# Kernel tuning notes

Hardware: AMD Instinct MI355X
Metric: run time of the kernel (lower is better)

## Reference

```python
import jax, jax.numpy as jnp
import numpy as np

B, N, H = 64, 512, 1024
NH = 8            # attention heads
HD = H // NH      # head dim
STEPS = 24


def setup_inputs() -> dict:
    key = jax.random.key(0)
    ks = jax.random.split(key, 12)
    s = 0.05  # weight scale to keep gates/softmax in a sane range
    return {
        "encoder_outputs": jax.random.normal(ks[0], (B, N, H), dtype=jnp.float32),
        "hidden": jax.random.normal(ks[1], (B, H), dtype=jnp.float32) * s,
        "cell": jax.random.normal(ks[2], (B, H), dtype=jnp.float32) * s,
        "end_node_embed": jax.random.normal(ks[3], (B, H), dtype=jnp.float32),
        "initial_input": jax.random.normal(ks[4], (B, 3 * H), dtype=jnp.float32),
        "max_steps": STEPS,
        # LSTMCell params (torch layout: [4H, in], gate order i,f,g,o)
        "W_ih": jax.random.normal(ks[5], (4 * H, 3 * H), dtype=jnp.float32) * s,
        "b_ih": jnp.zeros((4 * H,), jnp.float32),
        "W_hh": jax.random.normal(ks[6], (4 * H, H), dtype=jnp.float32) * s,
        "b_hh": jnp.zeros((4 * H,), jnp.float32),
        # MultiheadAttention params (torch in_proj [3H,H] = [Wq;Wk;Wv])
        "attn_in_w": jax.random.normal(ks[7], (3 * H, H), dtype=jnp.float32) * s,
        "attn_in_b": jnp.zeros((3 * H,), jnp.float32),
        "attn_out_w": jax.random.normal(ks[8], (H, H), dtype=jnp.float32) * s,
        "attn_out_b": jnp.zeros((H,), jnp.float32),
        # query_transform Linear
        "qt_w": jax.random.normal(ks[9], (H, H), dtype=jnp.float32) * s,
        "qt_b": jnp.zeros((H,), jnp.float32),
    }


def reference(encoder_outputs, hidden, cell, end_node_embed, initial_input,
              max_steps, W_ih, b_ih, W_hh, b_hh,
              attn_in_w, attn_in_b, attn_out_w, attn_out_b, qt_w, qt_b):
    b, n, h = encoder_outputs.shape
    nh, hd = NH, H // NH
    Wq, Wk, Wv = jnp.split(attn_in_w, 3, axis=0)
    bq, bk, bv = jnp.split(attn_in_b, 3)
    S = max_steps
    dt = encoder_outputs.dtype
    buf0 = jnp.zeros((b, S, h), dt)  # preallocated KV cache of decoder hiddens
    neg = jnp.asarray(-1e30, dt)
    scale = 1.0 / jnp.sqrt(jnp.asarray(hd, dt))
    pos = jnp.arange(S)

    def step(carry, t):
        hn, cn, x, buf = carry
        # --- LSTMCell (torch gate order i,f,g,o) ---
        gates = x @ W_ih.T + b_ih + hn @ W_hh.T + b_hh
        i, f, g, o = jnp.split(gates, 4, axis=-1)
        cn = jax.nn.sigmoid(f) * cn + jax.nn.sigmoid(i) * jnp.tanh(g)
        hn = jax.nn.sigmoid(o) * jnp.tanh(cn)
        buf = buf.at[:, t, :].set(hn)
        # --- causal self-attention: q = current hidden, kv = all hiddens <= t ---
        q = (hn @ Wq.T + bq).reshape(b, nh, hd)
        k = (buf @ Wk.T + bk).reshape(b, S, nh, hd)
        v = (buf @ Wv.T + bv).reshape(b, S, nh, hd)
        scores = jnp.einsum('bhd,bshd->bhs', q, k) * scale
        scores = jnp.where((pos > t)[None, None, :], neg, scores)
        attn = jax.nn.softmax(scores, axis=-1)
        ctx = jnp.einsum('bhs,bshd->bhd', attn, v).reshape(b, h)
        attn_out = ctx @ attn_out_w.T + attn_out_b
        # --- pointer scoring ---
        query = (0.5 * (hn + attn_out)) @ qt_w.T + qt_b
        logits = jnp.einsum('bh,bnh->bn', query, encoder_outputs)  # [B,N]
        _, idx = jax.lax.top_k(logits, 3)
        idx = jnp.sort(idx, axis=1)
        top3 = jnp.take_along_axis(encoder_outputs, idx[:, :, None], axis=1)  # [B,3,H]
        x = top3.reshape(b, 3 * h)
        return (hn, cn, x, buf), (logits, idx)

    _, (logits, idx) = jax.lax.scan(
        step, (hidden, cell, initial_input, buf0), jnp.arange(S))
    return logits, idx  # [max_steps,B,N], [max_steps,B,3]
```

## Files before the change

### kernel.cpp

```cpp
#include <hip/hip_runtime.h>
#include <math.h>

#define B_  64
#define N_  512
#define H_  1024
#define NH_ 8
#define HD_ 128
#define S_  24

__global__ __launch_bounds__(256) void wc_pre(
    const float* __restrict__ Wqt, const float* __restrict__ Wout,
    float* __restrict__ W2)
{
  __shared__ float As[16][68];
  __shared__ float Bs[16][68];
  const int tid = threadIdx.x;
  const int k0 = (blockIdx.x & 15) * 64;
  const int n0 = (blockIdx.x >> 4) * 64;
  const int tn = tid & 15, tm = tid >> 4;

#pragma unroll
  for (int i = 0; i < 4; ++i) {
    int n = n0 + tm * 4 + i;
    float4 w = *(const float4*)(Wqt + (size_t)n * 1024 + k0 + tn * 4);
    *(float4*)(W2 + (size_t)n * 2048 + k0 + tn * 4) =
        make_float4(0.5f * w.x, 0.5f * w.y, 0.5f * w.z, 0.5f * w.w);
  }

  float acc[4][4];
#pragma unroll
  for (int i = 0; i < 4; ++i)
#pragma unroll
    for (int j = 0; j < 4; ++j) acc[i][j] = 0.f;

  for (int m0 = 0; m0 < 1024; m0 += 16) {
    {
      int nn = tid >> 2, mm = (tid & 3) * 4;
      float4 a = *(const float4*)(Wqt + (size_t)(n0 + nn) * 1024 + m0 + mm);
      As[mm + 0][nn] = a.x; As[mm + 1][nn] = a.y;
      As[mm + 2][nn] = a.z; As[mm + 3][nn] = a.w;
      int mr = tid >> 4, kc = (tid & 15) * 4;
      float4 b = *(const float4*)(Wout + (size_t)(m0 + mr) * 1024 + k0 + kc);
      *(float4*)(&Bs[mr][kc]) = b;
    }
    __syncthreads();
#pragma unroll
    for (int m = 0; m < 16; ++m) {
      float av[4], bv[4];
      *(float4*)av = *(const float4*)(&As[m][tm * 4]);
      *(float4*)bv = *(const float4*)(&Bs[m][tn * 4]);
#pragma unroll
      for (int i = 0; i < 4; ++i)
#pragma unroll
        for (int j = 0; j < 4; ++j)
          acc[i][j] = fmaf(av[i], bv[j], acc[i][j]);
    }
    __syncthreads();
  }
#pragma unroll
  for (int i = 0; i < 4; ++i) {
    int n = n0 + tm * 4 + i;
    *(float4*)(W2 + (size_t)n * 2048 + 1024 + k0 + tn * 4) =
        make_float4(0.5f * acc[i][0], 0.5f * acc[i][1],
                    0.5f * acc[i][2], 0.5f * acc[i][3]);
  }
}

__global__ __launch_bounds__(256) void bc_pre(
    const float* __restrict__ Wqt, const float* __restrict__ bout,
    const float* __restrict__ bqt, float* __restrict__ bc)
{
  int w = threadIdx.x >> 6, lane = threadIdx.x & 63;
  int n = blockIdx.x * 4 + w;
  const float* row = Wqt + (size_t)n * 1024;
  float s = 0.f;
#pragma unroll
  for (int c = 0; c < 4; ++c) {
    float4 a = *(const float4*)(row + lane * 16 + c * 4);
    float4 b = *(const float4*)(bout + lane * 16 + c * 4);
    s = fmaf(a.x, b.x, fmaf(a.y, b.y, fmaf(a.z, b.z, fmaf(a.w, b.w, s))));
  }
#pragma unroll
  for (int off = 32; off > 0; off >>= 1) s += __shfl_down(s, off, 64);
  if (lane == 0) bc[n] = 0.5f * s + bqt[n];
}

__global__ __launch_bounds__(512, 2) void gemm5(
    const float* __restrict__ A0, int ldA0, const float* __restrict__ W0, int ldW0,
    int K0,
    const float* __restrict__ A1, int ldA1, const float* __restrict__ W1, int ldW1,
    const float* __restrict__ enc, const int* __restrict__ idxi, int gather,
    float* __restrict__ P, int N, int KS)
{
  __shared__ float As[16 * 68];
  __shared__ float Bs[16 * 132];
  const int tid = threadIdx.x;
  const int nb = blockIdx.x, sp = blockIdx.y;
  const int ks = sp * KS;

  const float* A; const float* W; int ldA, ldW, koff; int seg0;
  if (ks < K0) { A = A0; W = W0; ldA = ldA0; ldW = ldW0; koff = ks; seg0 = 1; }
  else { A = A1; W = W1; ldA = ldA1; ldW = ldW1; koff = ks - K0; seg0 = 0; }

  const int tn = tid & 31, tm = tid >> 5;
  const int lr = tid >> 2, lc = (tid & 3) * 4;

  float acc[4][4];
#pragma unroll
  for (int i = 0; i < 4; ++i)
#pragma unroll
    for (int j = 0; j < 4; ++j) acc[i][j] = 0.f;

  const float* Wrow = W + (size_t)(nb * 128 + lr) * ldW + koff + lc;
  const float* Arow = nullptr;
  if (tid < 256) {
    if (seg0 && gather) {
      int ei = idxi[lr * 3 + (koff >> 10)];
      Arow = enc + ((size_t)lr * 512 + ei) * 1024 + (koff & 1023) + lc;
    } else {
      Arow = A + (size_t)lr * ldA + koff + lc;
    }
  }

  for (int k0 = 0; k0 < KS; k0 += 16) {
    float4 b4 = *(const float4*)(Wrow + k0);
    if (tid < 256) {
      float4 a4 = *(const float4*)(Arow + k0);
      As[(lc + 0) * 68 + lr] = a4.x; As[(lc + 1) * 68 + lr] = a4.y;
      As[(lc + 2) * 68 + lr] = a4.z; As[(lc + 3) * 68 + lr] = a4.w;
    }
    Bs[(lc + 0) * 132 + lr] = b4.x; Bs[(lc + 1) * 132 + lr] = b4.y;
    Bs[(lc + 2) * 132 + lr] = b4.z; Bs[(lc + 3) * 132 + lr] = b4.w;
    __syncthreads();
#pragma unroll
    for (int k = 0; k < 16; ++k) {
      float av[4], bv[4];
      *(float4*)av = *(const float4*)(As + k * 68 + tm * 4);
      *(float4*)bv = *(const float4*)(Bs + k * 132 + tn * 4);
#pragma unroll
      for (int i = 0; i < 4; ++i)
#pragma unroll
        for (int j = 0; j < 4; ++j)
          acc[i][j] = fmaf(av[i], bv[j], acc[i][j]);
    }
    __syncthreads();
  }
  float* Pb = P + (size_t)sp * 64 * N + nb * 128;
#pragma unroll
  for (int i = 0; i < 4; ++i)
    *(float4*)(Pb + (size_t)(tm * 4 + i) * N + tn * 4) =
        make_float4(acc[i][0], acc[i][1], acc[i][2], acc[i][3]);
}

__device__ __forceinline__ float sigm(float x) { return 1.f / (1.f + expf(-x)); }

__global__ __launch_bounds__(256) void lstm_red(
    const float* __restrict__ P, const float* __restrict__ b_ih,
    const float* __restrict__ b_hh, const float* __restrict__ c_in,
    float* __restrict__ h_out, float* __restrict__ c_out)
{
  int idx = blockIdx.x * 256 + threadIdx.x;
  int b = idx >> 8, j4 = (idx & 255) * 4;
  float g[4][4];
#pragma unroll
  for (int c = 0; c < 4; ++c) {
    int n = c * 1024 + j4;
    float4 s = *(const float4*)(b_ih + n);
    float4 s2 = *(const float4*)(b_hh + n);
    s.x += s2.x; s.y += s2.y; s.z += s2.z; s.w += s2.w;
#pragma unroll
    for (int sp = 0; sp < 8; ++sp) {
      float4 v = *(const float4*)(P + ((size_t)sp * 64 + b) * 4096 + n);
      s.x += v.x; s.y += v.y; s.z += v.z; s.w += v.w;
    }
    g[c][0] = s.x; g[c][1] = s.y; g[c][2] = s.z; g[c][3] = s.w;
  }
  float4 cp = *(const float4*)(c_in + b * 1024 + j4);
  float cv[4] = {cp.x, cp.y, cp.z, cp.w};
  float4 ho, co;
  float* hp = &ho.x; float* cpn = &co.x;
#pragma unroll
  for (int e = 0; e < 4; ++e) {
    float c = sigm(g[1][e]) * cv[e] + sigm(g[0][e]) * tanhf(g[2][e]);
    cpn[e] = c;
    hp[e] = sigm(g[3][e]) * tanhf(c);
  }
  *(float4*)(c_out + b * 1024 + j4) = co;
  *(float4*)(h_out + b * 1024 + j4) = ho;
}

__global__ __launch_bounds__(128) void attn_fused(
    const float* __restrict__ P, const float* __restrict__ bqkv,
    float* __restrict__ Kc, float* __restrict__ Vc,
    float* __restrict__ ctx, int t)
{
  const float scale = 0.08838834764831845f;
  int bh = blockIdx.x;
  int b = bh >> 3, h = bh & 7;
  int d = threadIdx.x;
  __shared__ float qs[128];
  __shared__ float sc[S_];

  const float* Pb = P + (size_t)b * 3072 + h * 128 + d;
  float qv = bqkv[h * 128 + d];
  float kv = bqkv[1024 + h * 128 + d];
  float vv = bqkv[2048 + h * 128 + d];
#pragma unroll
  for (int sp = 0; sp < 8; ++sp) {
    const float* pp = Pb + (size_t)sp * 64 * 3072;
    qv += pp[0]; kv += pp[1024]; vv += pp[2048];
  }
  float* Kb = Kc + (size_t)(b * NH_ + h) * S_ * HD_;
  float* Vb = Vc + (size_t)(b * NH_ + h) * S_ * HD_;
  Kb[t * 128 + d] = kv;
  Vb[t * 128 + d] = vv;
  qs[d] = qv;
  __syncthreads();

  int wave = d >> 6, lane = d & 63;
  for (int s = wave; s <= t; s += 2) {
    float pr = qs[lane] * Kb[s * 128 + lane] + qs[lane + 64] * Kb[s * 128 + lane + 64];
#pragma unroll
    for (int off = 32; off > 0; off >>= 1) pr += __shfl_down(pr, off, 64);
    if (lane == 0) sc[s] = pr * scale;
  }
  __syncthreads();

  float m = -3.4e38f;
  for (int s = 0; s <= t; ++s) m = fmaxf(m, sc[s]);
  float den = 0.f;
  for (int s = 0; s <= t; ++s) den += expf(sc[s] - m);
  float acc = 0.f;
  for (int s = 0; s <= t; ++s) acc += expf(sc[s] - m) * Vb[s * 128 + d];
  ctx[(size_t)b * 1024 + h * 128 + d] = acc / den;
}

__device__ __forceinline__ void ins3(float v, int i,
    float& v0, int& i0, float& v1, int& i1, float& v2, int& i2)
{
  if (v > v0 || (v == v0 && i < i0)) {
    v2 = v1; i2 = i1; v1 = v0; i1 = i0; v0 = v; i0 = i;
  } else if (v > v1 || (v == v1 && i < i1)) {
    v2 = v1; i2 = i1; v1 = v; i1 = i;
  } else if (v > v2 || (v == v2 && i < i2)) {
    v2 = v; i2 = i;
  }
}

__global__ __launch_bounds__(512) void logits3(
    const float* __restrict__ P, const float* __restrict__ bc,
    const float* __restrict__ enc, float* __restrict__ out,
    float* __restrict__ candv, int* __restrict__ candi)
{
  __shared__ float qs[1024];
  __shared__ float cv[24];
  __shared__ int   ci[24];
  const int tid = threadIdx.x;
  const int b = blockIdx.x >> 3, ng = blockIdx.x & 7;

  if (tid < 256) {
    const int j4 = tid * 4;
    float4 s = *(const float4*)(bc + j4);
#pragma unroll
    for (int sp = 0; sp < 16; ++sp) {
      float4 v = *(const float4*)(P + ((size_t)sp * 64 + b) * 1024 + j4);
      s.x += v.x; s.y += v.y; s.z += v.z; s.w += v.w;
    }
    *(float4*)(qs + j4) = s;
  }
  __syncthreads();

  const int wave = tid >> 6, lane = tid & 63;
  float4 q0 = *(const float4*)(qs + lane * 4);
  float4 q1 = *(const float4*)(qs + 256 + lane * 4);
  float4 q2 = *(const float4*)(qs + 512 + lane * 4);
  float4 q3 = *(const float4*)(qs + 768 + lane * 4);

  const int row0 = ng * 64 + wave * 8;
  const float* eb = enc + ((size_t)b * N_ + row0) * 1024 + lane * 4;
  float* lo = out + (size_t)b * N_ + row0;
  float v0 = -3.4e38f, v1 = -3.4e38f, v2 = -3.4e38f;
  int i0 = 0x7fffffff, i1 = 0x7fffffff, i2 = 0x7fffffff;
  float myout = 0.f;
#pragma unroll 4
  for (int r = 0; r < 8; ++r) {
    const float* e = eb + (size_t)r * 1024;
    float4 e0 = *(const float4*)(e);
    float4 e1 = *(const float4*)(e + 256);
    float4 e2 = *(const float4*)(e + 512);
    float4 e3 = *(const float4*)(e + 768);
    float s = 0.f;
    s = fmaf(q0.x, e0.x, s); s = fmaf(q0.y, e0.y, s);
    s = fmaf(q0.z, e0.z, s); s = fmaf(q0.w, e0.w, s);
    s = fmaf(q1.x, e1.x, s); s = fmaf(q1.y, e1.y, s);
    s = fmaf(q1.z, e1.z, s); s = fmaf(q1.w, e1.w, s);
    s = fmaf(q2.x, e2.x, s); s = fmaf(q2.y, e2.y, s);
    s = fmaf(q2.z, e2.z, s); s = fmaf(q2.w, e2.w, s);
    s = fmaf(q3.x, e3.x, s); s = fmaf(q3.y, e3.y, s);
    s = fmaf(q3.z, e3.z, s); s = fmaf(q3.w, e3.w, s);
#pragma unroll
    for (int off = 32; off > 0; off >>= 1) s += __shfl_xor(s, off, 64);
    if (lane == r) myout = s;
    ins3(s, row0 + r, v0, i0, v1, i1, v2, i2);
  }
  if (lane < 8) lo[lane] = myout;
  if (lane == 0) {
    cv[wave * 3 + 0] = v0; ci[wave * 3 + 0] = i0;
    cv[wave * 3 + 1] = v1; ci[wave * 3 + 1] = i1;
    cv[wave * 3 + 2] = v2; ci[wave * 3 + 2] = i2;
  }
  __syncthreads();
  if (tid == 0) {
    float w0 = -3.4e38f, w1 = -3.4e38f, w2 = -3.4e38f;
    int j0 = 0x7fffffff, j1 = 0x7fffffff, j2 = 0x7fffffff;
#pragma unroll
    for (int k = 0; k < 24; ++k)
      ins3(cv[k], ci[k], w0, j0, w1, j1, w2, j2);
    candv[blockIdx.x * 3 + 0] = w0; candi[blockIdx.x * 3 + 0] = j0;
    candv[blockIdx.x * 3 + 1] = w1; candi[blockIdx.x * 3 + 1] = j1;
    candv[blockIdx.x * 3 + 2] = w2; candi[blockIdx.x * 3 + 2] = j2;
  }
}

__global__ __launch_bounds__(64) void top3_merge(
    const float* __restrict__ candv, const int* __restrict__ candi,
    float* __restrict__ idx_out, int* __restrict__ idxi)
{
  int b = threadIdx.x;
  float v0 = -3.4e38f, v1 = -3.4e38f, v2 = -3.4e38f;
  int i0 = 0x7fffffff, i1 = 0x7fffffff, i2 = 0x7fffffff;
#pragma unroll
  for (int q = 0; q < 8; ++q) {
    int base = (b * 8 + q) * 3;
#pragma unroll
    for (int k = 0; k < 3; ++k)
      ins3(candv[base + k], candi[base + k], v0, i0, v1, i1, v2, i2);
  }
  int a = i0, bb = i1, c = i2, tw;
  if (a > bb) { tw = a; a = bb; bb = tw; }
  if (bb > c) { tw = bb; bb = c; c = tw; }
  if (a > bb) { tw = a; a = bb; bb = tw; }
  idxi[b * 3 + 0] = a; idxi[b * 3 + 1] = bb; idxi[b * 3 + 2] = c;
  idx_out[b * 3 + 0] = (float)a;
  idx_out[b * 3 + 1] = (float)bb;
  idx_out[b * 3 + 2] = (float)c;
}

extern "C" void kernel_launch(void* const* d_in, const int* in_sizes, int n_in,
                              void* d_out, int out_size, void* d_ws, size_t ws_size,
                              hipStream_t stream)
{
  (void)in_sizes; (void)n_in; (void)out_size; (void)ws_size;
  const float* enc   = (const float*)d_in[0];
  const float* h0    = (const float*)d_in[1];
  const float* c0    = (const float*)d_in[2];
  const float* x0    = (const float*)d_in[4];
  const float* W_ih  = (const float*)d_in[6];
  const float* b_ih  = (const float*)d_in[7];
  const float* W_hh  = (const float*)d_in[8];
  const float* b_hh  = (const float*)d_in[9];
  const float* Wqkv  = (const float*)d_in[10];
  const float* bqkv  = (const float*)d_in[11];
  const float* Wout  = (const float*)d_in[12];
  const float* bout  = (const float*)d_in[13];
  const float* Wqt   = (const float*)d_in[14];
  const float* bqt   = (const float*)d_in[15];

  float* ws   = (float*)d_ws;
  float* P    = ws;
  float* W2   = P + 8 * 64 * 4096;
  float* bc   = W2 + 1024 * 2048;
  float* hbuf = bc + 1024;
  float* cbuf = hbuf + 64 * 1024;
  float* ctx  = cbuf + 64 * 1024;
  float* Kc   = ctx + 64 * 1024;
  float* Vc   = Kc + 64 * NH_ * S_ * HD_;
  float* candv = Vc + 64 * NH_ * S_ * HD_;
  int*   candi = (int*)(candv + 512 * 3);
  int*   idxi  = candi + 512 * 3;

  float* logits_out = (float*)d_out;
  float* idx_out    = logits_out + (size_t)S_ * B_ * N_;

  wc_pre<<<dim3(256), dim3(256), 0, stream>>>(Wqt, Wout, W2);
  bc_pre<<<dim3(256), dim3(256), 0, stream>>>(Wqt, bout, bqt, bc);

  for (int t = 0; t < S_; ++t) {
    const float* xin   = (t == 0) ? x0 : nullptr;
    const float* hprev = (t == 0) ? h0 : hbuf;
    const float* cprev = (t == 0) ? c0 : cbuf;

    gemm5<<<dim3(32, 8), dim3(512), 0, stream>>>(
        xin, 3072, W_ih, 3072, 3072,
        hprev, 1024, W_hh, 1024,
        enc, idxi, t > 0, P, 4096, 512);
    lstm_red<<<dim3(64), dim3(256), 0, stream>>>(P, b_ih, b_hh, cprev, hbuf, cbuf);

    gemm5<<<dim3(24, 8), dim3(512), 0, stream>>>(
        hbuf, 1024, Wqkv, 1024, 1024,
        hbuf, 1024, Wqkv, 1024,
        enc, idxi, 0, P, 3072, 128);
    attn_fused<<<dim3(512), dim3(128), 0, stream>>>(P, bqkv, Kc, Vc, ctx, t);

    gemm5<<<dim3(8, 16), dim3(512), 0, stream>>>(
        hbuf, 1024, W2, 2048, 1024,
        ctx, 1024, W2 + 1024, 2048,
        enc, idxi, 0, P, 1024, 128);
    logits3<<<dim3(512), dim3(512), 0, stream>>>(
        P, bc, enc, logits_out + (size_t)t * B_ * N_, candv, candi);
    top3_merge<<<dim3(1), dim3(64), 0, stream>>>(
        candv, candi, idx_out + (size_t)t * B_ * 3, idxi);
  }
}
```

Before: 3.742 ms.

## Fuse LSTM reduction and top-3 merge into preceding kernels via last-block counters

The LSTM gate reduction is folded into the gate GEMM. W rows are permuted so that each column block holds all four gates for 32 hidden units, and the last split-K block to arrive, found with an atomic counter, does the reduction and cell update. The top-3 merge likewise moves into the last-finishing logits3 block, the bias precompute is merged into wc_pre, and h is double-buffered. This removes three kernel launches per step plus one at setup, at the cost of atomics, threadfences and a serial tail in one block.

Result: slower. 6.767 ms (+80.9%).

```diff
diff --git a/kernel.cpp b/kernel.cpp
--- a/kernel.cpp
+++ b/kernel.cpp
@@ -10,8 +10,12 @@
 
 __global__ __launch_bounds__(256) void wc_pre(
     const float* __restrict__ Wqt, const float* __restrict__ Wout,
-    float* __restrict__ W2)
-{
+    const float* __restrict__ bout, const float* __restrict__ bqt,
+    float* __restrict__ W2, float* __restrict__ bc,
+    unsigned* __restrict__ cnts)
+{
+  if (blockIdx.x == 0 && threadIdx.x < 33) cnts[threadIdx.x] = 0u;
+
   __shared__ float As[16][68];
   __shared__ float Bs[16][68];
   const int tid = threadIdx.x;
@@ -64,43 +68,57 @@
         make_float4(0.5f * acc[i][0], 0.5f * acc[i][1],
                     0.5f * acc[i][2], 0.5f * acc[i][3]);
   }
-}
-
-__global__ __launch_bounds__(256) void bc_pre(
-    const float* __restrict__ Wqt, const float* __restrict__ bout,
-    const float* __restrict__ bqt, float* __restrict__ bc)
-{
-  int w = threadIdx.x >> 6, lane = threadIdx.x & 63;
-  int n = blockIdx.x * 4 + w;
-  const float* row = Wqt + (size_t)n * 1024;
-  float s = 0.f;
-#pragma unroll
-  for (int c = 0; c < 4; ++c) {
-    float4 a = *(const float4*)(row + lane * 16 + c * 4);
-    float4 b = *(const float4*)(bout + lane * 16 + c * 4);
-    s = fmaf(a.x, b.x, fmaf(a.y, b.y, fmaf(a.z, b.z, fmaf(a.w, b.w, s))));
-  }
-#pragma unroll
-  for (int off = 32; off > 0; off >>= 1) s += __shfl_down(s, off, 64);
-  if (lane == 0) bc[n] = 0.5f * s + bqt[n];
-}
-
-__global__ __launch_bounds__(512, 2) void gemm5(
-    const float* __restrict__ A0, int ldA0, const float* __restrict__ W0, int ldW0,
-    int K0,
-    const float* __restrict__ A1, int ldA1, const float* __restrict__ W1, int ldW1,
+
+  {
+    int w = tid >> 6, lane = tid & 63;
+    int n = blockIdx.x * 4 + w;
+    const float* row = Wqt + (size_t)n * 1024;
+    float s = 0.f;
+#pragma unroll
+    for (int c = 0; c < 4; ++c) {
+      float4 a = *(const float4*)(row + lane * 16 + c * 4);
+      float4 b = *(const float4*)(bout + lane * 16 + c * 4);
+      s = fmaf(a.x, b.x, fmaf(a.y, b.y, fmaf(a.z, b.z, fmaf(a.w, b.w, s))));
+    }
+#pragma unroll
+    for (int off = 32; off > 0; off >>= 1) s += __shfl_down(s, off, 64);
+    if (lane == 0) bc[n] = 0.5f * s + bqt[n];
+  }
+}
+
+__device__ __forceinline__ float sigm(float x) { return 1.f / (1.f + expf(-x)); }
+
+__device__ __forceinline__ void ins3(float v, int i,
+    float& v0, int& i0, float& v1, int& i1, float& v2, int& i2)
+{
+  if (v > v0 || (v == v0 && i < i0)) {
+    v2 = v1; i2 = i1; v1 = v0; i1 = i0; v0 = v; i0 = i;
+  } else if (v > v1 || (v == v1 && i < i1)) {
+    v2 = v1; i2 = i1; v1 = v; i1 = i;
+  } else if (v > v2 || (v == v2 && i < i2)) {
+    v2 = v; i2 = i;
+  }
+}
+
+__global__ __launch_bounds__(512, 2) void gemm_gates(
+    const float* __restrict__ x0, const float* __restrict__ h_prev,
+    const float* __restrict__ W_ih, const float* __restrict__ W_hh,
     const float* __restrict__ enc, const int* __restrict__ idxi, int gather,
-    float* __restrict__ P, int N, int KS)
+    const float* __restrict__ b_ih, const float* __restrict__ b_hh,
+    const float* __restrict__ c_in, float* __restrict__ c_out,
+    float* __restrict__ h_out, float* __restrict__ P,
+    unsigned* __restrict__ cnt, int step)
 {
   __shared__ float As[16 * 68];
   __shared__ float Bs[16 * 132];
+  __shared__ int amLast;
   const int tid = threadIdx.x;
   const int nb = blockIdx.x, sp = blockIdx.y;
-  const int ks = sp * KS;
+  const int ks = sp * 512;
 
   const float* A; const float* W; int ldA, ldW, koff; int seg0;
-  if (ks < K0) { A = A0; W = W0; ldA = ldA0; ldW = ldW0; koff = ks; seg0 = 1; }
-  else { A = A1; W = W1; ldA = ldA1; ldW = ldW1; koff = ks - K0; seg0 = 0; }
+  if (ks < 3072) { W = W_ih; ldW = 3072; koff = ks; A = x0;     ldA = 3072; seg0 = 1; }
+  else           { W = W_hh; ldW = 1024; koff = ks - 3072; A = h_prev; ldA = 1024; seg0 = 0; }
 
   const int tn = tid & 31, tm = tid >> 5;
   const int lr = tid >> 2, lc = (tid & 3) * 4;
@@ -111,7 +129,8 @@
 #pragma unroll
     for (int j = 0; j < 4; ++j) acc[i][j] = 0.f;
 
-  const float* Wrow = W + (size_t)(nb * 128 + lr) * ldW + koff + lc;
+  const int wrow = (lr >> 5) * 1024 + nb * 32 + (lr & 31);
+  const float* Wrow = W + (size_t)wrow * ldW + koff + lc;
   const float* Arow = nullptr;
   if (tid < 256) {
     if (seg0 && gather) {
@@ -122,6 +141,101 @@
     }
   }
 
+  for (int k0 = 0; k0 < 512; k0 += 16) {
+    float4 b4 = *(const float4*)(Wrow + k0);
+    if (tid < 256) {
+      float4 a4 = *(const float4*)(Arow + k0);
+      As[(lc + 0) * 68 + lr] = a4.x; As[(lc + 1) * 68 + lr] = a4.y;
+      As[(lc + 2) * 68 + lr] = a4.z; As[(lc + 3) * 68 + lr] = a4.w;
+    }
+    Bs[(lc + 0) * 132 + lr] = b4.x; Bs[(lc + 1) * 132 + lr] = b4.y;
+    Bs[(lc + 2) * 132 + lr] = b4.z; Bs[(lc + 3) * 132 + lr] = b4.w;
+    __syncthreads();
+#pragma unroll
+    for (int k = 0; k < 16; ++k) {
+      float av[4], bv[4];
+      *(float4*)av = *(const float4*)(As + k * 68 + tm * 4);
+      *(float4*)bv = *(const float4*)(Bs + k * 132 + tn * 4);
+#pragma unroll
+      for (int i = 0; i < 4; ++i)
+#pragma unroll
+        for (int j = 0; j < 4; ++j)
+          acc[i][j] = fmaf(av[i], bv[j], acc[i][j]);
+    }
+    __syncthreads();
+  }
+  float* Pb = P + (size_t)sp * 64 * 4096 + nb * 128;
+#pragma unroll
+  for (int i = 0; i < 4; ++i)
+    *(float4*)(Pb + (size_t)(tm * 4 + i) * 4096 + tn * 4) =
+        make_float4(acc[i][0], acc[i][1], acc[i][2], acc[i][3]);
+
+  __threadfence();
+  __syncthreads();
+  if (tid == 0) {
+    unsigned old = atomicAdd(&cnt[nb], 1u);
+    amLast = (old == (unsigned)(step * 8 + 7));
+  }
+  __syncthreads();
+  if (!amLast) return;
+  __threadfence();
+
+  const int b = tid >> 3, j4 = (tid & 7) * 4;
+  const int jg = nb * 32 + j4;
+  float g[4][4];
+#pragma unroll
+  for (int gi = 0; gi < 4; ++gi) {
+    float4 s  = *(const float4*)(b_ih + gi * 1024 + jg);
+    float4 s2 = *(const float4*)(b_hh + gi * 1024 + jg);
+    s.x += s2.x; s.y += s2.y; s.z += s2.z; s.w += s2.w;
+    const int lcb = nb * 128 + gi * 32 + j4;
+#pragma unroll
+    for (int spp = 0; spp < 8; ++spp) {
+      float4 v = *(const float4*)(P + ((size_t)spp * 64 + b) * 4096 + lcb);
+      s.x += v.x; s.y += v.y; s.z += v.z; s.w += v.w;
+    }
+    g[gi][0] = s.x; g[gi][1] = s.y; g[gi][2] = s.z; g[gi][3] = s.w;
+  }
+  float4 cp = *(const float4*)(c_in + b * 1024 + jg);
+  float cv[4] = {cp.x, cp.y, cp.z, cp.w};
+  float4 ho, co; float* hp = &ho.x; float* cpn = &co.x;
+#pragma unroll
+  for (int e = 0; e < 4; ++e) {
+    float c = sigm(g[1][e]) * cv[e] + sigm(g[0][e]) * tanhf(g[2][e]);
+    cpn[e] = c; hp[e] = sigm(g[3][e]) * tanhf(c);
+  }
+  *(float4*)(c_out + b * 1024 + jg) = co;
+  *(float4*)(h_out + b * 1024 + jg) = ho;
+}
+
+__global__ __launch_bounds__(512, 2) void gemm5(
+    const float* __restrict__ A0, int ldA0, const float* __restrict__ W0, int ldW0,
+    int K0,
+    const float* __restrict__ A1, int ldA1, const float* __restrict__ W1, int ldW1,
+    float* __restrict__ P, int N, int KS)
+{
+  __shared__ float As[16 * 68];
+  __shared__ float Bs[16 * 132];
+  const int tid = threadIdx.x;
+  const int nb = blockIdx.x, sp = blockIdx.y;
+  const int ks = sp * KS;
+
+  const float* A; const float* W; int ldA, ldW, koff;
+  if (ks < K0) { A = A0; W = W0; ldA = ldA0; ldW = ldW0; koff = ks; }
+  else { A = A1; W = W1; ldA = ldA1; ldW = ldW1; koff = ks - K0; }
+
+  const int tn = tid & 31, tm = tid >> 5;
+  const int lr = tid >> 2, lc = (tid & 3) * 4;
+
+  float acc[4][4];
+#pragma unroll
+  for (int i = 0; i < 4; ++i)
+#pragma unroll
+    for (int j = 0; j < 4; ++j) acc[i][j] = 0.f;
+
+  const float* Wrow = W + (size_t)(nb * 128 + lr) * ldW + koff + lc;
+  const float* Arow = (tid < 256) ? A + (size_t)lr * ldA + koff + lc : nullptr;
+
   for (int k0 = 0; k0 < KS; k0 += 16) {
     float4 b4 = *(const float4*)(Wrow + k0);
     if (tid < 256) {
@@ -150,43 +264,6 @@
   for (int i = 0; i < 4; ++i)
     *(float4*)(Pb + (size_t)(tm * 4 + i) * N + tn * 4) =
         make_float4(acc[i][0], acc[i][1], acc[i][2], acc[i][3]);
-}
-
-__device__ __forceinline__ float sigm(float x) { return 1.f / (1.f + expf(-x)); }
-
-__global__ __launch_bounds__(256) void lstm_red(
-    const float* __restrict__ P, const float* __restrict__ b_ih,
-    const float* __restrict__ b_hh, const float* __restrict__ c_in,
-    float* __restrict__ h_out, float* __restrict__ c_out)
-{
-  int idx = blockIdx.x * 256 + threadIdx.x;
-  int b = idx >> 8, j4 = (idx & 255) * 4;
-  float g[4][4];
-#pragma unroll
-  for (int c = 0; c < 4; ++c) {
-    int n = c * 1024 + j4;
-    float4 s = *(const float4*)(b_ih + n);
-    float4 s2 = *(const float4*)(b_hh + n);
-    s.x += s2.x; s.y += s2.y; s.z += s2.z; s.w += s2.w;
-#pragma unroll
-    for (int sp = 0; sp < 8; ++sp) {
-      float4 v = *(const float4*)(P + ((size_t)sp * 64 + b) * 4096 + n);
-      s.x += v.x; s.y += v.y; s.z += v.z; s.w += v.w;
-    }
-    g[c][0] = s.x; g[c][1] = s.y; g[c][2] = s.z; g[c][3] = s.w;
-  }
-  float4 cp = *(const float4*)(c_in + b * 1024 + j4);
-  float cv[4] = {cp.x, cp.y, cp.z, cp.w};
-  float4 ho, co;
-  float* hp = &ho.x; float* cpn = &co.x;
-#pragma unroll
-  for (int e = 0; e < 4; ++e) {
-    float c = sigm(g[1][e]) * cv[e] + sigm(g[0][e]) * tanhf(g[2][e]);
-    cpn[e] = c;
-    hp[e] = sigm(g[3][e]) * tanhf(c);
-  }
-  *(float4*)(c_out + b * 1024 + j4) = co;
-  *(float4*)(h_out + b * 1024 + j4) = ho;
 }
 
 __global__ __launch_bounds__(128) void attn_fused(
@@ -235,26 +312,17 @@
   ctx[(size_t)b * 1024 + h * 128 + d] = acc / den;
 }
 
-__device__ __forceinline__ void ins3(float v, int i,
-    float& v0, int& i0, float& v1, int& i1, float& v2, int& i2)
-{
-  if (v > v0 || (v == v0 && i < i0)) {
-    v2 = v1; i2 = i1; v1 = v0; i1 = i0; v0 = v; i0 = i;
-  } else if (v > v1 || (v == v1 && i < i1)) {
-    v2 = v1; i2 = i1; v1 = v; i1 = i;
-  } else if (v > v2 || (v == v2 && i < i2)) {
-    v2 = v; i2 = i;
-  }
-}
-
 __global__ __launch_bounds__(512) void logits3(
     const float* __restrict__ P, const float* __restrict__ bc,
     const float* __restrict__ enc, float* __restrict__ out,
-    float* __restrict__ candv, int* __restrict__ candi)
+    float* __restrict__ candv, int* __restrict__ candi,
+    unsigned* __restrict__ cntL, int step,
+    int* __restrict__ idxi, float* __restrict__ idx_out)
 {
   __shared__ float qs[1024];
   __shared__ float cv[24];
   __shared__ int   ci[24];
+  __shared__ int   amLast;
   const int tid = threadIdx.x;
   const int b = blockIdx.x >> 3, ng = blockIdx.x & 7;
 
@@ -320,30 +388,35 @@
     candv[blockIdx.x * 3 + 1] = w1; candi[blockIdx.x * 3 + 1] = j1;
     candv[blockIdx.x * 3 + 2] = w2; candi[blockIdx.x * 3 + 2] = j2;
   }
-}
-
-__global__ __launch_bounds__(64) void top3_merge(
-    const float* __restrict__ candv, const int* __restrict__ candi,
-    float* __restrict__ idx_out, int* __restrict__ idxi)
-{
-  int b = threadIdx.x;
-  float v0 = -3.4e38f, v1 = -3.4e38f, v2 = -3.4e38f;
-  int i0 = 0x7fffffff, i1 = 0x7fffffff, i2 = 0x7fffffff;
-#pragma unroll
-  for (int q = 0; q < 8; ++q) {
-    int base = (b * 8 + q) * 3;
-#pragma unroll
-    for (int k = 0; k < 3; ++k)
-      ins3(candv[base + k], candi[base + k], v0, i0, v1, i1, v2, i2);
-  }
-  int a = i0, bb = i1, c = i2, tw;
-  if (a > bb) { tw = a; a = bb; bb = tw; }
-  if (bb > c) { tw = bb; bb = c; c = tw; }
-  if (a > bb) { tw = a; a = bb; bb = tw; }
-  idxi[b * 3 + 0] = a; idxi[b * 3 + 1] = bb; idxi[b * 3 + 2] = c;
-  idx_out[b * 3 + 0] = (float)a;
-  idx_out[b * 3 + 1] = (float)bb;
-  idx_out[b * 3 + 2] = (float)c;
+
+  __threadfence();
+  __syncthreads();
+  if (tid == 0) {
+    unsigned old = atomicAdd(cntL, 1u);
+    amLast = (old == (unsigned)(step * 512 + 511));
+  }
+  __syncthreads();
+  if (!amLast) return;
+  __threadfence();
+  if (tid < 64) {
+    const int bb_ = tid;
+    float w0 = -3.4e38f, w1 = -3.4e38f, w2 = -3.4e38f;
+    int j0 = 0x7fffffff, j1 = 0x7fffffff, j2 = 0x7fffffff;
+#pragma unroll
+    for (int q = 0; q < 8; ++q) {
+      int base = (bb_ * 8 + q) * 3;
+#pragma unroll
+      for (int k = 0; k < 3; ++k)
+        ins3(candv[base + k], candi[base + k], w0, j0, w1, j1, w2, j2);
+    }
+    int a = j0, bb = j1, c = j2, tw;
+    if (a > bb) { tw = a; a = bb; bb = tw; }
+    if (bb > c) { tw = bb; bb = c; c = tw; }
+    if (a > bb) { tw = a; a = bb; bb = tw; }
+    idxi[bb_ * 3 + 0] = a; idxi[bb_ * 3 + 1] = bb; idxi[bb_ * 3 + 2] = c;
+    float* io = idx_out + bb_ * 3;
+    io[0] = (float)a; io[1] = (float)bb; io[2] = (float)c;
+  }
 }
 
 extern "C" void kernel_launch(void* const* d_in, const int* in_sizes, int n_in,
@@ -366,49 +439,48 @@
   const float* Wqt   = (const float*)d_in[14];
   const float* bqt   = (const float*)d_in[15];
 
-  float* ws   = (float*)d_ws;
-  float* P    = ws;
-  float* W2   = P + 8 * 64 * 4096;
-  float* bc   = W2 + 1024 * 2048;
-  float* hbuf = bc + 1024;
-  float* cbuf = hbuf + 64 * 1024;
-  float* ctx  = cbuf + 64 * 1024;
-  float* Kc   = ctx + 64 * 1024;
-  float* Vc   = Kc + 64 * NH_ * S_ * HD_;
+  float* ws    = (float*)d_ws;
+  float* P     = ws;
+  float* W2    = P + 8 * 64 * 4096;
+  float* bc    = W2 + 1024 * 2048;
+  float* hbuf  = bc + 1024;
+  float* hbuf2 = hbuf + 64 * 1024;
+  float* cbuf  = hbuf2 + 64 * 1024;
+  float* ctx   = cbuf + 64 * 1024;
+  float* Kc    = ctx + 64 * 1024;
+  float* Vc    = Kc + 64 * NH_ * S_ * HD_;
   float* candv = Vc + 64 * NH_ * S_ * HD_;
   int*   candi = (int*)(candv + 512 * 3);
   int*   idxi  = candi + 512 * 3;
+  unsigned* cnt = (unsigned*)(idxi + 192);
 
   float* logits_out = (float*)d_out;
   float* idx_out    = logits_out + (size_t)S_ * B_ * N_;
 
-  wc_pre<<<dim3(256), dim3(256), 0, stream>>>(Wqt, Wout, W2);
-  bc_pre<<<dim3(256), dim3(256), 0, stream>>>(Wqt, bout, bqt, bc);
+  wc_pre<<<dim3(256), dim3(256), 0, stream>>>(Wqt, Wout, bout, bqt, W2, bc, cnt);
 
   for (int t = 0; t < S_; ++t) {
-    const float* xin   = (t == 0) ? x0 : nullptr;
-    const float* hprev = (t == 0) ? h0 : hbuf;
+    float* hnew = (t & 1) ? hbuf2 : hbuf;
+    const float* hprev = (t == 0) ? h0 : ((t & 1) ? hbuf : hbuf2);
     const float* cprev = (t == 0) ? c0 : cbuf;
 
-    gemm5<<<dim3(32, 8), dim3(512), 0, stream>>>(
-        xin, 3072, W_ih, 3072, 3072,
-        hprev, 1024, W_hh, 1024,
-        enc, idxi, t > 0, P, 4096, 512);
-    lstm_red<<<dim3(64), dim3(256), 0, stream>>>(P, b_ih, b_hh, cprev, hbuf, cbuf);
+    gemm_gates<<<dim3(32, 8), dim3(512), 0, stream>>>(
+        x0, hprev, W_ih, W_hh, enc, idxi, t > 0,
+        b_ih, b_hh, cprev, cbuf, hnew, P, cnt, t);
 
     gemm5<<<dim3(24, 8), dim3(512), 0, stream>>>(
-        hbuf, 1024, Wqkv, 1024, 1024,
-        hbuf, 1024, Wqkv, 1024,
-        enc, idxi, 0, P, 3072, 128);
+        hnew, 1024, Wqkv, 1024, 1024,
+        hnew, 1024, Wqkv, 1024,
+        P, 3072, 128);
     attn_fused<<<dim3(512), dim3(128), 0, stream>>>(P, bqkv, Kc, Vc, ctx, t);
 
     gemm5<<<dim3(8, 16), dim3(512), 0, stream>>>(
-        hbuf, 1024, W2, 2048, 1024,
+        hnew, 1024, W2, 2048, 1024,
         ctx, 1024, W2 + 1024, 2048,
-        enc, idxi, 0, P, 1024, 128);
+        P, 1024, 128);
+
     logits3<<<dim3(512), dim3(512), 0, stream>>>(
-        P, bc, enc, logits_out + (size_t)t * B_ * N_, candv, candi);
-    top3_merge<<<dim3(1), dim3(64), 0, stream>>>(
-        candv, candi, idx_out + (size_t)t * B_ * 3, idxi);
-  }
-}
+        P, bc, enc, logits_out + (size_t)t * B_ * N_, candv, candi,
+        cnt + 32, t, idxi, idx_out + (size_t)t * B_ * 3);
+  }
+}
```

## Fuse top-3 merge into next-step gates GEMM and split logits into smaller blocks

Applied to the files above, without the earlier changes.

Removes the per-step single-block top3_merge launch by having each gates-GEMM block recompute the top-3 merge from the candidate buffers, with one block also writing the previous step's indices. Merges bc_pre into wc_pre. Doubles the logits grid to 1024 blocks of 256 threads, each covering 32 rows, and processes two rows per iteration for more memory-level parallelism. This trades a tiny serial kernel per step for redundant 48-candidate merges inside many GEMM threads, which adds branchy work at GEMM start.

After: 5.124 ms. +36.9%, slower.

```diff
diff --git a/kernel.cpp b/kernel.cpp
--- a/kernel.cpp
+++ b/kernel.cpp
@@ -10,7 +10,8 @@
 
 __global__ __launch_bounds__(256) void wc_pre(
     const float* __restrict__ Wqt, const float* __restrict__ Wout,
-    float* __restrict__ W2)
+    const float* __restrict__ bout, const float* __restrict__ bqt,
+    float* __restrict__ W2, float* __restrict__ bc)
 {
   __shared__ float As[16][68];
   __shared__ float Bs[16][68];
@@ -64,32 +65,136 @@
         make_float4(0.5f * acc[i][0], 0.5f * acc[i][1],
                     0.5f * acc[i][2], 0.5f * acc[i][3]);
   }
-}
-
-__global__ __launch_bounds__(256) void bc_pre(
-    const float* __restrict__ Wqt, const float* __restrict__ bout,
-    const float* __restrict__ bqt, float* __restrict__ bc)
-{
-  int w = threadIdx.x >> 6, lane = threadIdx.x & 63;
-  int n = blockIdx.x * 4 + w;
-  const float* row = Wqt + (size_t)n * 1024;
-  float s = 0.f;
-#pragma unroll
-  for (int c = 0; c < 4; ++c) {
-    float4 a = *(const float4*)(row + lane * 16 + c * 4);
-    float4 b = *(const float4*)(bout + lane * 16 + c * 4);
-    s = fmaf(a.x, b.x, fmaf(a.y, b.y, fmaf(a.z, b.z, fmaf(a.w, b.w, s))));
-  }
-#pragma unroll
-  for (int off = 32; off > 0; off >>= 1) s += __shfl_down(s, off, 64);
-  if (lane == 0) bc[n] = 0.5f * s + bqt[n];
+
+  {
+    int w = tid >> 6, lane = tid & 63;
+    int n = blockIdx.x * 4 + w;
+    const float* row = Wqt + (size_t)n * 1024;
+    float s = 0.f;
+#pragma unroll
+    for (int c = 0; c < 4; ++c) {
+      float4 a = *(const float4*)(row + lane * 16 + c * 4);
+      float4 b = *(const float4*)(bout + lane * 16 + c * 4);
+      s = fmaf(a.x, b.x, fmaf(a.y, b.y, fmaf(a.z, b.z, fmaf(a.w, b.w, s))));
+    }
+#pragma unroll
+    for (int off = 32; off > 0; off >>= 1) s += __shfl_down(s, off, 64);
+    if (lane == 0) bc[n] = 0.5f * s + bqt[n];
+  }
+}
+
+__device__ __forceinline__ float sigm(float x) { return 1.f / (1.f + expf(-x)); }
+
+__device__ __forceinline__ void ins3(float v, int i,
+    float& v0, int& i0, float& v1, int& i1, float& v2, int& i2)
+{
+  if (v > v0 || (v == v0 && i < i0)) {
+    v2 = v1; i2 = i1; v1 = v0; i1 = i0; v0 = v; i0 = i;
+  } else if (v > v1 || (v == v1 && i < i1)) {
+    v2 = v1; i2 = i1; v1 = v; i1 = i;
+  } else if (v > v2 || (v == v2 && i < i2)) {
+    v2 = v; i2 = i;
+  }
+}
+
+__device__ __forceinline__ void merge_top3(
+    const float* __restrict__ candv, const int* __restrict__ candi,
+    int b, int& a, int& bb, int& c)
+{
+  float v0 = -3.4e38f, v1 = -3.4e38f, v2 = -3.4e38f;
+  int i0 = 0x7fffffff, i1 = 0x7fffffff, i2 = 0x7fffffff;
+  const int base = b * 48;
+#pragma unroll
+  for (int k = 0; k < 48; ++k)
+    ins3(candv[base + k], candi[base + k], v0, i0, v1, i1, v2, i2);
+  a = i0; bb = i1; c = i2;
+  int tw;
+  if (a > bb) { tw = a; a = bb; bb = tw; }
+  if (bb > c) { tw = bb; bb = c; c = tw; }
+  if (a > bb) { tw = a; a = bb; bb = tw; }
+}
+
+__global__ __launch_bounds__(512, 2) void gemm_gates(
+    const float* __restrict__ x0, const float* __restrict__ h_prev,
+    const float* __restrict__ W_ih, const float* __restrict__ W_hh,
+    const float* __restrict__ enc,
+    const float* __restrict__ candv, const int* __restrict__ candi, int gather,
+    float* __restrict__ P, float* __restrict__ idx_out_prev)
+{
+  __shared__ float As[16 * 68];
+  __shared__ float Bs[16 * 132];
+  const int tid = threadIdx.x;
+  const int nb = blockIdx.x, sp = blockIdx.y;
+  const int ks = sp * 512;
+
+  const float* A; const float* W; int ldA, ldW, koff; int seg0;
+  if (ks < 3072) { A = x0; W = W_ih; ldA = 3072; ldW = 3072; koff = ks; seg0 = 1; }
+  else { A = h_prev; W = W_hh; ldA = 1024; ldW = 1024; koff = ks - 3072; seg0 = 0; }
+
+  const int tn = tid & 31, tm = tid >> 5;
+  const int lr = tid >> 2, lc = (tid & 3) * 4;
+
+  if (gather && nb == 0 && sp == 0 && tid < 64) {
+    int a, bb, c;
+    merge_top3(candv, candi, tid, a, bb, c);
+    float* io = idx_out_prev + tid * 3;
+    io[0] = (float)a; io[1] = (float)bb; io[2] = (float)c;
+  }
+
+  float acc[4][4];
+#pragma unroll
+  for (int i = 0; i < 4; ++i)
+#pragma unroll
+    for (int j = 0; j < 4; ++j) acc[i][j] = 0.f;
+
+  const float* Wrow = W + (size_t)(nb * 128 + lr) * ldW + koff + lc;
+  const float* Arow = nullptr;
+  if (tid < 256) {
+    if (seg0 && gather) {
+      int a, bb, c;
+      merge_top3(candv, candi, lr, a, bb, c);
+      const int g = koff >> 10;
+      const int ei = (g == 0) ? a : ((g == 1) ? bb : c);
+      Arow = enc + ((size_t)lr * 512 + ei) * 1024 + (koff & 1023) + lc;
+    } else {
+      Arow = A + (size_t)lr * ldA + koff + lc;
+    }
+  }
+
+  for (int k0 = 0; k0 < 512; k0 += 16) {
+    float4 b4 = *(const float4*)(Wrow + k0);
+    if (tid < 256) {
+      float4 a4 = *(const float4*)(Arow + k0);
+      As[(lc + 0) * 68 + lr] = a4.x; As[(lc + 1) * 68 + lr] = a4.y;
+      As[(lc + 2) * 68 + lr] = a4.z; As[(lc + 3) * 68 + lr] = a4.w;
+    }
+    Bs[(lc + 0) * 132 + lr] = b4.x; Bs[(lc + 1) * 132 + lr] = b4.y;
+    Bs[(lc + 2) * 132 + lr] = b4.z; Bs[(lc + 3) * 132 + lr] = b4.w;
+    __syncthreads();
+#pragma unroll
+    for (int k = 0; k < 16; ++k) {
+      float av[4], bv[4];
+      *(float4*)av = *(const float4*)(As + k * 68 + tm * 4);
+      *(float4*)bv = *(const float4*)(Bs + k * 132 + tn * 4);
+#pragma unroll
+      for (int i = 0; i < 4; ++i)
+#pragma unroll
+        for (int j = 0; j < 4; ++j)
+          acc[i][j] = fmaf(av[i], bv[j], acc[i][j]);
+    }
+    __syncthreads();
+  }
+  float* Pb = P + (size_t)sp * 64 * 4096 + nb * 128;
+#pragma unroll
+  for (int i = 0; i < 4; ++i)
+    *(float4*)(Pb + (size_t)(tm * 4 + i) * 4096 + tn * 4) =
+        make_float4(acc[i][0], acc[i][1], acc[i][2], acc[i][3]);
 }
 
 __global__ __launch_bounds__(512, 2) void gemm5(
     const float* __restrict__ A0, int ldA0, const float* __restrict__ W0, int ldW0,
     int K0,
     const float* __restrict__ A1, int ldA1, const float* __restrict__ W1, int ldW1,
-    const float* __restrict__ enc, const int* __restrict__ idxi, int gather,
     float* __restrict__ P, int N, int KS)
 {
   __shared__ float As[16 * 68];
@@ -98,9 +203,9 @@
   const int nb = blockIdx.x, sp = blockIdx.y;
   const int ks = sp * KS;
 
-  const float* A; const float* W; int ldA, ldW, koff; int seg0;
-  if (ks < K0) { A = A0; W = W0; ldA = ldA0; ldW = ldW0; koff = ks; seg0 = 1; }
-  else { A = A1; W = W1; ldA = ldA1; ldW = ldW1; koff = ks - K0; seg0 = 0; }
+  const float* A; const float* W; int ldA, ldW, koff;
+  if (ks < K0) { A = A0; W = W0; ldA = ldA0; ldW = ldW0; koff = ks; }
+  else { A = A1; W = W1; ldA = ldA1; ldW = ldW1; koff = ks - K0; }
 
   const int tn = tid & 31, tm = tid >> 5;
   const int lr = tid >> 2, lc = (tid & 3) * 4;
@@ -112,15 +217,7 @@
     for (int j = 0; j < 4; ++j) acc[i][j] = 0.f;
 
   const float* Wrow = W + (size_t)(nb * 128 + lr) * ldW + koff + lc;
-  const float* Arow = nullptr;
-  if (tid < 256) {
-    if (seg0 && gather) {
-      int ei = idxi[lr * 3 + (koff >> 10)];
-      Arow = enc + ((size_t)lr * 512 + ei) * 1024 + (koff & 1023) + lc;
-    } else {
-      Arow = A + (size_t)lr * ldA + koff + lc;
-    }
-  }
+  const float* Arow = (tid < 256) ? A + (size_t)lr * ldA + koff + lc : nullptr;
 
   for (int k0 = 0; k0 < KS; k0 += 16) {
     float4 b4 = *(const float4*)(Wrow + k0);
@@ -151,8 +248,6 @@
     *(float4*)(Pb + (size_t)(tm * 4 + i) * N + tn * 4) =
         make_float4(acc[i][0], acc[i][1], acc[i][2], acc[i][3]);
 }
-
-__device__ __forceinline__ float sigm(float x) { return 1.f / (1.f + expf(-x)); }
 
 __global__ __launch_bounds__(256) void lstm_red(
     const float* __restrict__ P, const float* __restrict__ b_ih,
@@ -235,30 +330,18 @@
   ctx[(size_t)b * 1024 + h * 128 + d] = acc / den;
 }
 
-__device__ __forceinline__ void ins3(float v, int i,
-    float& v0, int& i0, float& v1, int& i1, float& v2, int& i2)
-{
-  if (v > v0 || (v == v0 && i < i0)) {
-    v2 = v1; i2 = i1; v1 = v0; i1 = i0; v0 = v; i0 = i;
-  } else if (v > v1 || (v == v1 && i < i1)) {
-    v2 = v1; i2 = i1; v1 = v; i1 = i;
-  } else if (v > v2 || (v == v2 && i < i2)) {
-    v2 = v; i2 = i;
-  }
-}
-
-__global__ __launch_bounds__(512) void logits3(
+__global__ __launch_bounds__(256) void logits4(
     const float* __restrict__ P, const float* __restrict__ bc,
     const float* __restrict__ enc, float* __restrict__ out,
     float* __restrict__ candv, int* __restrict__ candi)
 {
   __shared__ float qs[1024];
-  __shared__ float cv[24];
-  __shared__ int   ci[24];
+  __shared__ float cv[12];
+  __shared__ int   ci[12];
   const int tid = threadIdx.x;
-  const int b = blockIdx.x >> 3, ng = blockIdx.x & 7;
-
-  if (tid < 256) {
+  const int b = blockIdx.x >> 4, ng = blockIdx.x & 15;
+
+  {
     const int j4 = tid * 4;
     float4 s = *(const float4*)(bc + j4);
 #pragma unroll
@@ -276,32 +359,50 @@
   float4 q2 = *(const float4*)(qs + 512 + lane * 4);
   float4 q3 = *(const float4*)(qs + 768 + lane * 4);
 
-  const int row0 = ng * 64 + wave * 8;
+  const int row0 = ng * 32 + wave * 8;
   const float* eb = enc + ((size_t)b * N_ + row0) * 1024 + lane * 4;
   float* lo = out + (size_t)b * N_ + row0;
   float v0 = -3.4e38f, v1 = -3.4e38f, v2 = -3.4e38f;
   int i0 = 0x7fffffff, i1 = 0x7fffffff, i2 = 0x7fffffff;
   float myout = 0.f;
-#pragma unroll 4
-  for (int r = 0; r < 8; ++r) {
-    const float* e = eb + (size_t)r * 1024;
-    float4 e0 = *(const float4*)(e);
-    float4 e1 = *(const float4*)(e + 256);
-    float4 e2 = *(const float4*)(e + 512);
-    float4 e3 = *(const float4*)(e + 768);
-    float s = 0.f;
-    s = fmaf(q0.x, e0.x, s); s = fmaf(q0.y, e0.y, s);
-    s = fmaf(q0.z, e0.z, s); s = fmaf(q0.w, e0.w, s);
-    s = fmaf(q1.x, e1.x, s); s = fmaf(q1.y, e1.y, s);
-    s = fmaf(q1.z, e1.z, s); s = fmaf(q1.w, e1.w, s);
-    s = fmaf(q2.x, e2.x, s); s = fmaf(q2.y, e2.y, s);
-    s = fmaf(q2.z, e2.z, s); s = fmaf(q2.w, e2.w, s);
-    s = fmaf(q3.x, e3.x, s); s = fmaf(q3.y, e3.y, s);
-    s = fmaf(q3.z, e3.z, s); s = fmaf(q3.w, e3.w, s);
-#pragma unroll
-    for (int off = 32; off > 0; off >>= 1) s += __shfl_xor(s, off, 64);
-    if (lane == r) myout = s;
-    ins3(s, row0 + r, v0, i0, v1, i1, v2, i2);
+#pragma unroll
+  for (int r = 0; r < 8; r += 2) {
+    const float* ea = eb + (size_t)r * 1024;
+    const float* eb2 = eb + (size_t)(r + 1) * 1024;
+    float4 a0 = *(const float4*)(ea);
+    float4 a1 = *(const float4*)(ea + 256);
+    float4 a2 = *(const float4*)(ea + 512);
+    float4 a3 = *(const float4*)(ea + 768);
+    float4 b0 = *(const float4*)(eb2);
+    float4 b1 = *(const float4*)(eb2 + 256);
+    float4 b2 = *(const float4*)(eb2 + 512);
+    float4 b3 = *(const float4*)(eb2 + 768);
+    float s0 = 0.f, s1 = 0.f;
+    s0 = fmaf(q0.x, a0.x, s0); s1 = fmaf(q0.x, b0.x, s1);
+    s0 = fmaf(q0.y, a0.y, s0); s1 = fmaf(q0.y, b0.y, s1);
+    s0 = fmaf(q0.z, a0.z, s0); s1 = fmaf(q0.z, b0.z, s1);
+    s0 = fmaf(q0.w, a0.w, s0); s1 = fmaf(q0.w, b0.w, s1);
+    s0 = fmaf(q1.x, a1.x, s0); s1 = fmaf(q1.x, b1.x, s1);
+    s0 = fmaf(q1.y, a1.y, s0); s1 = fmaf(q1.y, b1.y, s1);
+    s0 = fmaf(q1.z, a1.z, s0); s1 = fmaf(q1.z, b1.z, s1);
+    s0 = fmaf(q1.w, a1.w, s0); s1 = fmaf(q1.w, b1.w, s1);
+    s0 = fmaf(q2.x, a2.x, s0); s1 = fmaf(q2.x, b2.x, s1);
+    s0 = fmaf(q2.y, a2.y, s0); s1 = fmaf(q2.y, b2.y, s1);
+    s0 = fmaf(q2.z, a2.z, s0); s1 = fmaf(q2.z, b2.z, s1);
+    s0 = fmaf(q2.w, a2.w, s0); s1 = fmaf(q2.w, b2.w, s1);
+    s0 = fmaf(q3.x, a3.x, s0); s1 = fmaf(q3.x, b3.x, s1);
+    s0 = fmaf(q3.y, a3.y, s0); s1 = fmaf(q3.y, b3.y, s1);
+    s0 = fmaf(q3.z, a3.z, s0); s1 = fmaf(q3.z, b3.z, s1);
+    s0 = fmaf(q3.w, a3.w, s0); s1 = fmaf(q3.w, b3.w, s1);
+#pragma unroll
+    for (int off = 32; off > 0; off >>= 1) {
+      s0 += __shfl_xor(s0, off, 64);
+      s1 += __shfl_xor(s1, off, 64);
+    }
+    if (lane == r) myout = s0;
+    if (lane == r + 1) myout = s1;
+    ins3(s0, row0 + r, v0, i0, v1, i1, v2, i2);
+    ins3(s1, row0 + r + 1, v0, i0, v1, i1, v2, i2);
   }
   if (lane < 8) lo[lane] = myout;
   if (lane == 0) {
@@ -314,7 +415,7 @@
     float w0 = -3.4e38f, w1 = -3.4e38f, w2 = -3.4e38f;
     int j0 = 0x7fffffff, j1 = 0x7fffffff, j2 = 0x7fffffff;
 #pragma unroll
-    for (int k = 0; k < 24; ++k)
+    for (int k = 0; k < 12; ++k)
       ins3(cv[k], ci[k], w0, j0, w1, j1, w2, j2);
     candv[blockIdx.x * 3 + 0] = w0; candi[blockIdx.x * 3 + 0] = j0;
     candv[blockIdx.x * 3 + 1] = w1; candi[blockIdx.x * 3 + 1] = j1;
@@ -322,25 +423,13 @@
   }
 }
 
-__global__ __launch_bounds__(64) void top3_merge(
+__global__ __launch_bounds__(64) void top3_final(
     const float* __restrict__ candv, const int* __restrict__ candi,
-    float* __restrict__ idx_out, int* __restrict__ idxi)
+    float* __restrict__ idx_out)
 {
   int b = threadIdx.x;
-  float v0 = -3.4e38f, v1 = -3.4e38f, v2 = -3.4e38f;
-  int i0 = 0x7fffffff, i1 = 0x7fffffff, i2 = 0x7fffffff;
-#pragma unroll
-  for (int q = 0; q < 8; ++q) {
-    int base = (b * 8 + q) * 3;
-#pragma unroll
-    for (int k = 0; k < 3; ++k)
-      ins3(candv[base + k], candi[base + k], v0, i0, v1, i1, v2, i2);
-  }
-  int a = i0, bb = i1, c = i2, tw;
-  if (a > bb) { tw = a; a = bb; bb = tw; }
-  if (bb > c) { tw = bb; bb = c; c = tw; }
-  if (a > bb) { tw = a; a = bb; bb = tw; }
-  idxi[b * 3 + 0] = a; idxi[b * 3 + 1] = bb; idxi[b * 3 + 2] = c;
+  int a, bb, c;
+  merge_top3(candv, candi, b, a, bb, c);
   idx_out[b * 3 + 0] = (float)a;
   idx_out[b * 3 + 1] = (float)bb;
   idx_out[b * 3 + 2] = (float)c;
@@ -366,49 +455,46 @@
   const float* Wqt   = (const float*)d_in[14];
   const float* bqt   = (const float*)d_in[15];
 
-  float* ws   = (float*)d_ws;
-  float* P    = ws;
-  float* W2   = P + 8 * 64 * 4096;
-  float* bc   = W2 + 1024 * 2048;
-  float* hbuf = bc + 1024;
-  float* cbuf = hbuf + 64 * 1024;
-  float* ctx  = cbuf + 64 * 1024;
-  float* Kc   = ctx + 64 * 1024;
-  float* Vc   = Kc + 64 * NH_ * S_ * HD_;
+  float* ws    = (float*)d_ws;
+  float* P     = ws;
+  float* W2    = P + 8 * 64 * 4096;
+  float* bc    = W2 + 1024 * 2048;
+  float* hbuf  = bc + 1024;
+  float* cbuf  = hbuf + 64 * 1024;
+  float* ctx   = cbuf + 64 * 1024;
+  float* Kc    = ctx + 64 * 1024;
+  float* Vc    = Kc + 64 * NH_ * S_ * HD_;
   float* candv = Vc + 64 * NH_ * S_ * HD_;
-  int*   candi = (int*)(candv + 512 * 3);
-  int*   idxi  = candi + 512 * 3;
+  int*   candi = (int*)(candv + 1024 * 3);
 
   float* logits_out = (float*)d_out;
   float* idx_out    = logits_out + (size_t)S_ * B_ * N_;
 
-  wc_pre<<<dim3(256), dim3(256), 0, stream>>>(Wqt, Wout, W2);
-  bc_pre<<<dim3(256), dim3(256), 0, stream>>>(Wqt, bout, bqt, bc);
+  wc_pre<<<dim3(256), dim3(256), 0, stream>>>(Wqt, Wout, bout, bqt, W2, bc);
 
   for (int t = 0; t < S_; ++t) {
-    const float* xin   = (t == 0) ? x0 : nullptr;
     const float* hprev = (t == 0) ? h0 : hbuf;
     const float* cprev = (t == 0) ? c0 : cbuf;
 
-    gemm5<<<dim3(32, 8), dim3(512), 0, stream>>>(
-        xin, 3072, W_ih, 3072, 3072,
-        hprev, 1024, W_hh, 1024,
-        enc, idxi, t > 0, P, 4096, 512);
+    gemm_gates<<<dim3(32, 8), dim3(512), 0, stream>>>(
+        x0, hprev, W_ih, W_hh, enc, candv, candi, t > 0, P,
+        (t > 0) ? idx_out + (size_t)(t - 1) * B_ * 3 : nullptr);
     lstm_red<<<dim3(64), dim3(256), 0, stream>>>(P, b_ih, b_hh, cprev, hbuf, cbuf);
 
     gemm5<<<dim3(24, 8), dim3(512), 0, stream>>>(
         hbuf, 1024, Wqkv, 1024, 1024,
         hbuf, 1024, Wqkv, 1024,
-        enc, idxi, 0, P, 3072, 128);
+        P, 3072, 128);
     attn_fused<<<dim3(512), dim3(128), 0, stream>>>(P, bqkv, Kc, Vc, ctx, t);
 
     gemm5<<<dim3(8, 16), dim3(512), 0, stream>>>(
         hbuf, 1024, W2, 2048, 1024,
         ctx, 1024, W2 + 1024, 2048,
-        enc, idxi, 0, P, 1024, 128);
-    logits3<<<dim3(512), dim3(512), 0, stream>>>(
+        P, 1024, 128);
+
+    logits4<<<dim3(1024), dim3(256), 0, stream>>>(
         P, bc, enc, logits_out + (size_t)t * B_ * N_, candv, candi);
-    top3_merge<<<dim3(1), dim3(64), 0, stream>>>(
-        candv, candi, idx_out + (size_t)t * B_ * 3, idxi);
-  }
-}
+  }
+  top3_final<<<dim3(1), dim3(64), 0, stream>>>(
+      candv, candi, idx_out + (size_t)(S_ - 1) * B_ * 3);
+}
```
